# Optimization experiments

Hardware: AMD Instinct MI355X
Metric: run time of the kernel (lower is better)

## Reference

```python
import jax, jax.numpy as jnp
import numpy as np

E = 384      # hidden_dim
H = 8        # num_attention_heads
D = E // H   # head_dim = 48


def setup_inputs() -> dict:
    key = jax.random.key(0)
    ks = jax.random.split(key, 11)
    B, S = 4, 2048
    patch_embeds = jax.random.normal(ks[0], (B, S, E), dtype=jnp.float32)
    attention_mask = jax.random.randint(ks[1], (B, S), 0, 2).astype(bool)
    s = 1.0 / np.sqrt(E)
    Wq = jax.random.normal(ks[2], (E, E), dtype=jnp.float32) * s
    bq = jnp.zeros((E,), dtype=jnp.float32)
    Wk = jax.random.normal(ks[3], (E, E), dtype=jnp.float32) * s
    bk = jnp.zeros((E,), dtype=jnp.float32)
    Wv = jax.random.normal(ks[4], (E, E), dtype=jnp.float32) * s
    bv = jnp.zeros((E,), dtype=jnp.float32)
    Wo = jax.random.normal(ks[5], (E, E), dtype=jnp.float32) * s
    bo = jnp.zeros((E,), dtype=jnp.float32)
    return {"patch_embeds": patch_embeds, "attention_mask": attention_mask,
            "Wq": Wq, "bq": bq, "Wk": Wk, "bk": bk,
            "Wv": Wv, "bv": bv, "Wo": Wo, "bo": bo}


def reference(patch_embeds, attention_mask, Wq, bq, Wk, bk, Wv, bv, Wo, bo):
    B, S, _ = patch_embeds.shape
    scale = D ** (-0.5)
    # QKV projections (nn.Linear: x @ W.T + b); W stored as [out,in]
    q = patch_embeds @ Wq.T + bq
    k = patch_embeds @ Wk.T + bk
    v = patch_embeds @ Wv.T + bv
    # [B,S,E] -> [B,H,S,D]
    q = q.reshape(B, S, H, D).transpose(0, 2, 1, 3)
    k = k.reshape(B, S, H, D).transpose(0, 2, 1, 3)
    v = v.reshape(B, S, H, D).transpose(0, 2, 1, 3)
    # scaled dot-product attention with key mask (True = masked)
    scores = jnp.einsum('bhqd,bhkd->bhqk', q, k) * scale
    mask = attention_mask[:, None, None, :]  # [B,1,1,S]
    scores = jnp.where(mask, -jnp.inf, scores)
    weights = jax.nn.softmax(scores, axis=-1)
    out = jnp.einsum('bhqk,bhkd->bhqd', weights, v)
    out = out.transpose(0, 2, 1, 3).reshape(B, S, E)
    return out @ Wo.T + bo
```

## Files before the change

### kernel.cpp

```cpp
#include <hip/hip_runtime.h>
#include <math.h>

#define B_ 4
#define S_ 2048
#define E_ 384
#define H_ 8
#define D_ 48
#define M_ (B_*S_)
#define DP_ 64
constexpr float QK_SCALE = 0.14433756729740643f * 1.4426950408889634f;

typedef __attribute__((ext_vector_type(8))) short short8;
typedef __attribute__((ext_vector_type(4))) float f32x4;
typedef __attribute__((ext_vector_type(4))) unsigned uint4v;
typedef unsigned short u16;

__device__ inline u16 f2bf(float f) {
    unsigned u = __float_as_uint(f);
    return (u16)((u + 0x7FFFu + ((u >> 16) & 1u)) >> 16);
}
__device__ inline float bf2f(u16 h) { return __uint_as_float(((unsigned)h) << 16); }
__device__ inline unsigned pk2(float a, float b) {
    return (unsigned)f2bf(a) | ((unsigned)f2bf(b) << 16);
}
__device__ inline unsigned pk2_fast(float a, float b) {
#if __has_builtin(__builtin_amdgcn_perm)
    unsigned ua = __float_as_uint(a) + 0x8000u;
    unsigned ub = __float_as_uint(b) + 0x8000u;
    return __builtin_amdgcn_perm(ub, ua, 0x07060302u);
#else
    return pk2(a, b);
#endif
}
__device__ inline float fexp2(float x) {
#if __has_builtin(__builtin_amdgcn_exp2f)
    return __builtin_amdgcn_exp2f(x);
#else
    return exp2f(x);
#endif
}
__device__ inline void glld16(const void* g, void* l) {
    __builtin_amdgcn_global_load_lds((const __attribute__((address_space(1))) unsigned int*)g,
                                     (__attribute__((address_space(3))) unsigned int*)l, 16, 0, 0);
}
__device__ inline void plswap32(unsigned &a, unsigned &b) {
#if __has_builtin(__builtin_amdgcn_permlane32_swap)
    auto r = __builtin_amdgcn_permlane32_swap(a, b, false, false);
    a = r[0]; b = r[1];
#else
    asm volatile("v_permlane32_swap_b32 %0, %1" : "+v"(a), "+v"(b));
#endif
}
__device__ inline void plswap16(unsigned &a, unsigned &b) {
#if __has_builtin(__builtin_amdgcn_permlane16_swap)
    auto r = __builtin_amdgcn_permlane16_swap(a, b, false, false);
    a = r[0]; b = r[1];
#else
    asm volatile("v_permlane16_swap_b32 %0, %1" : "+v"(a), "+v"(b));
#endif
}

__global__ __launch_bounds__(256) void prep(const float4* __restrict__ x,
                                            const int* __restrict__ mask,
                                            const float4* __restrict__ wq,
                                            const float4* __restrict__ wk,
                                            const float4* __restrict__ wv,
                                            const float4* __restrict__ wo,
                                            uint2* __restrict__ xb,
                                            uint2* __restrict__ wb,
                                            u16* __restrict__ Qp, u16* __restrict__ Kp) {
    const int bx = blockIdx.x, t = threadIdx.x;
    if (bx < 3072) {
        int i = bx * 256 + t;
        float4 v = x[i];
        uint2 H;
        H.x = pk2(v.x, v.y);
        H.y = pk2(v.z, v.w);
        xb[i] = H;
    } else if (bx < 3072 + 144) {
        int i = (bx - 3072) * 256 + t;
        const int n4 = 36864;
        const float4* srcs[4] = {wq, wk, wv, wo};
        #pragma unroll
        for (int j = 0; j < 4; ++j) {
            float4 v = srcs[j][i];
            uint2 H;
            H.x = pk2(v.x, v.y);
            H.y = pk2(v.z, v.w);
            wb[(size_t)j * n4 + i] = H;
        }
    } else {
        int i = (bx - 3216) * 256 + t;
        int bh = i >> 11, s = i & 2047, b = bh >> 3;
        size_t off = ((size_t)bh * S_ + s) * DP_ + 48;
        uint4 qz = {0x00004300u, 0, 0, 0};
        uint4 kz = {mask[b * S_ + s] ? 0x0000BF80u : 0u, 0, 0, 0};
        uint4 z  = {0, 0, 0, 0};
        *reinterpret_cast<uint4*>(Qp + off)     = qz;
        *reinterpret_cast<uint4*>(Qp + off + 8) = z;
        *reinterpret_cast<uint4*>(Kp + off)     = kz;
        *reinterpret_cast<uint4*>(Kp + off + 8) = z;
    }
}

__global__ __launch_bounds__(256) void gemm_qkv3(const u16* __restrict__ xb,
                                                 const u16* __restrict__ wb,
                                                 const float* __restrict__ bq,
                                                 const float* __restrict__ bk,
                                                 const float* __restrict__ bv,
                                                 u16* __restrict__ Qp, u16* __restrict__ Kp,
                                                 u16* __restrict__ Vtp) {
    __shared__ u16 smem[4 * 4096];
    u16* As = smem;

    const int t = threadIdx.x, w = t >> 6, lane = t & 63;
    const int ln = lane & 15, quad = lane >> 4;
    const int gr = lane >> 3;
    const int gc = (lane & 7) ^ gr;
    const int m0 = blockIdx.x * 64;
    const int n0 = blockIdx.y * 64;
    const int b  = m0 >> 11;

    f32x4 acc[3][4];
    #pragma unroll
    for (int j = 0; j < 3; ++j)
        #pragma unroll
        for (int nt = 0; nt < 4; ++nt)
            acc[j][nt] = (f32x4){0.f, 0.f, 0.f, 0.f};

    for (int kk = 0; kk < 384; kk += 64) {
        __syncthreads();
        #pragma unroll
        for (int i = 0; i < 2; ++i) {
            int r0 = w * 16 + i * 8;
            glld16(xb + (size_t)(m0 + r0 + gr) * E_ + kk + gc * 8, As + r0 * 64);
        }
        #pragma unroll
        for (int j = 0; j < 3; ++j)
            #pragma unroll
            for (int i = 0; i < 2; ++i) {
                int r0 = w * 16 + i * 8;
                glld16(wb + (size_t)j * 147456 + (size_t)(n0 + r0 + gr) * E_ + kk + gc * 8,
                       smem + (1 + j) * 4096 + r0 * 64);
            }
        __syncthreads();

        #pragma unroll
        for (int ks = 0; ks < 2; ++ks) {
            const int slot = (ks * 4 + quad) ^ (ln & 7);
            short8 ah = *reinterpret_cast<const short8*>(&As[(w * 16 + ln) * 64 + slot * 8]);
            #pragma unroll
            for (int j = 0; j < 3; ++j) {
                const u16* Wsj = smem + (1 + j) * 4096;
                #pragma unroll
                for (int nt = 0; nt < 4; ++nt) {
                    short8 wf = *reinterpret_cast<const short8*>(&Wsj[(nt * 16 + ln) * 64 + slot * 8]);
                    acc[j][nt] = __builtin_amdgcn_mfma_f32_16x16x32_bf16(ah, wf, acc[j][nt], 0, 0, 0);
                }
            }
        }
    }

    {
        const int s_base = (m0 & 2047) + w * 16 + quad * 4;
        #pragma unroll
        for (int nt = 0; nt < 4; ++nt) {
            const int col = n0 + nt * 16 + ln;
            const int h   = (col * 683) >> 15;
            const int d   = col - h * 48;
            const float bc = bv[col];
            u16* dst = Vtp + ((size_t)(b * 8 + h) * 48 + d) * 2048;
            uint2 pk;
            pk.x = pk2(acc[2][nt][0] + bc, acc[2][nt][1] + bc);
            pk.y = pk2(acc[2][nt][2] + bc, acc[2][nt][3] + bc);
            *reinterpret_cast<uint2*>(dst + s_base) = pk;
        }
    }

    u16* TrQ = smem;
    u16* TrK = smem + 64 * 76;
    __syncthreads();
    #pragma unroll
    for (int nt = 0; nt < 4; ++nt) {
        const int col = n0 + nt * 16 + ln;
        const float bcq = bq[col], bck = bk[col];
        #pragma unroll
        for (int r = 0; r < 4; ++r) {
            int row = w * 16 + quad * 4 + r;
            TrQ[row * 76 + nt * 16 + ln] = f2bf((acc[0][nt][r] + bcq) * QK_SCALE);
            TrK[row * 76 + nt * 16 + ln] = f2bf(acc[1][nt][r] + bck);
        }
    }
    __syncthreads();
    {
        const int row = t >> 2, quarter = t & 3;
        const int s   = (m0 & 2047) + row;
        #pragma unroll
        for (int c = 0; c < 2; ++c) {
            int gcol = n0 + quarter * 16 + c * 8;
            int h = (gcol * 683) >> 15;
            int d = gcol - h * 48;
            size_t off = ((size_t)(b * 8 + h) * 2048 + s) * DP_ + d;
            *reinterpret_cast<uint4*>(Qp + off) =
                *reinterpret_cast<const uint4*>(&TrQ[row * 76 + quarter * 16 + c * 8]);
            *reinterpret_cast<uint4*>(Kp + off) =
                *reinterpret_cast<const uint4*>(&TrK[row * 76 + quarter * 16 + c * 8]);
        }
    }
}

__global__ __launch_bounds__(256) void gemm_out(const u16* __restrict__ ab,
                                                const u16* __restrict__ wb,
                                                const float* __restrict__ bo, float* __restrict__ out) {
    __shared__ u16 smem[2 * 4096 + 2 * 4096];
    u16* As = smem;
    u16* Ws = smem + 2 * 4096;
    const int t = threadIdx.x, w = t >> 6, lane = t & 63;
    const int ln = lane & 15, quad = lane >> 4;
    const int gr = lane >> 3;
    const int gc = (lane & 7) ^ gr;
    const int m0 = blockIdx.x * 64, n0 = blockIdx.y * 64;
    const u16* wh = wb + (size_t)3 * 147456;

    f32x4 acc[4];
    #pragma unroll
    for (int nt = 0; nt < 4; ++nt) acc[nt] = (f32x4){0.f, 0.f, 0.f, 0.f};

    auto stage = [&](int bf, int kk) {
        #pragma unroll
        for (int i = 0; i < 2; ++i) {
            int r0 = w * 16 + i * 8;
            glld16(ab + (size_t)(m0 + r0 + gr) * E_ + kk + gc * 8, As + bf * 4096 + r0 * 64);
            glld16(wh + (size_t)(n0 + r0 + gr) * E_ + kk + gc * 8, Ws + bf * 4096 + r0 * 64);
        }
    };

    stage(0, 0);
    __syncthreads();
    #pragma unroll
    for (int it = 0; it < 6; ++it) {
        const int cur = it & 1;
        if (it < 5) stage(cur ^ 1, (it + 1) * 64);
        const u16* Ab = As + cur * 4096;
        const u16* Wb = Ws + cur * 4096;
        #pragma unroll
        for (int ks = 0; ks < 2; ++ks) {
            const int slot = (ks * 4 + quad) ^ (ln & 7);
            short8 ah = *reinterpret_cast<const short8*>(&Ab[(w * 16 + ln) * 64 + slot * 8]);
            #pragma unroll
            for (int nt = 0; nt < 4; ++nt) {
                short8 wf = *reinterpret_cast<const short8*>(&Wb[(nt * 16 + ln) * 64 + slot * 8]);
                acc[nt] = __builtin_amdgcn_mfma_f32_16x16x32_bf16(ah, wf, acc[nt], 0, 0, 0);
            }
        }
        __syncthreads();
    }

    #pragma unroll
    for (int nt = 0; nt < 4; ++nt) {
        const int col = n0 + nt * 16 + ln;
        const float bc = bo[col];
        #pragma unroll
        for (int r = 0; r < 4; ++r) {
            size_t row = (size_t)(m0 + w * 16 + quad * 4 + r);
            out[row * E_ + col] = acc[nt][r] + bc;
        }
    }
}

__global__ __launch_bounds__(512, 4) void attn_mfma(const u16* __restrict__ Qp,
                                                    const u16* __restrict__ Kp,
                                                    const u16* __restrict__ Vtp,
                                                    u16* __restrict__ AO) {
    __shared__ __align__(16) u16 QPs[128 * 64];
    __shared__ __align__(16) u16 Ksh[2][128 * 64];
    __shared__ __align__(16) u16 Vt[2][48 * 128];
    __shared__ float linv[8][16];

    const int t    = threadIdx.x;
    const int w    = t >> 6;
    const int lane = t & 63;
    const int ln   = lane & 15;
    const int quad = lane >> 4;
    const int gr   = lane >> 3;
    const int gc   = (lane & 7) ^ gr;
    const int vr   = lane >> 4;
    const int vc   = lane & 15;
    const int bh   = blockIdx.x;
    const int q0   = blockIdx.y * 128;
    const int b    = bh >> 3, h = bh & 7;
    const int cb   = h * 48;
    const size_t rb = (size_t)b * S_;

    const u16* Qsrc = Qp  + ((size_t)bh * S_ + q0) * DP_;
    const u16* Ksrc = Kp  + (size_t)bh * S_ * DP_;
    const u16* Vsrc = Vtp + (size_t)bh * 48 * 2048;

    const int swz0 = ((quad    ) ^ (ln & 7)) << 3;
    const int swz1 = ((4 + quad) ^ (ln & 7)) << 3;
    const u16* kA[2][2];
    const u16* vA[2][4];
    #pragma unroll
    for (int bf = 0; bf < 2; ++bf) {
        kA[bf][0] = &Ksh[bf][ln * 64 + swz0];
        kA[bf][1] = &Ksh[bf][ln * 64 + swz1];
        #pragma unroll
        for (int g = 0; g < 4; ++g)
            vA[bf][g] = &Vt[bf][ln * 128 + (((g * 4 + quad) ^ (ln & 7)) << 3)];
    }
    const int qrow = (w * 16 + ln) * 64;
    const u16* pR[2];
    pR[0] = &QPs[qrow + swz0];
    pR[1] = &QPs[qrow + swz1];

    auto stage = [&](int bf, int kt) {
        const int k0 = kt * 128;
        #pragma unroll
        for (int i = 0; i < 2; ++i)
            glld16(Ksrc + (size_t)(k0 + w * 16 + i * 8 + gr) * DP_ + gc * 8,
                   &Ksh[bf][(w * 16 + i * 8) * 64]);
        if (w < 6) {
            #pragma unroll
            for (int j = 0; j < 2; ++j) {
                const int vrow = w * 8 + j * 4 + vr;
                glld16(Vsrc + (size_t)vrow * 2048 + k0 + (vc ^ (vrow & 7)) * 8,
                       &Vt[bf][(w * 8 + j * 4) * 128]);
            }
        }
    };

    #pragma unroll
    for (int i = 0; i < 2; ++i) {
        int r0 = w * 16 + i * 8;
        glld16(Qsrc + (size_t)(r0 + gr) * DP_ + gc * 8, &QPs[r0 * 64]);
    }
    stage(0, 0);
    __syncthreads();

    short8 qf[2];
    qf[0] = *reinterpret_cast<const short8*>(pR[0]);
    qf[1] = *reinterpret_cast<const short8*>(pR[1]);

    f32x4 o[3];
    #pragma unroll
    for (int nt = 0; nt < 3; ++nt) o[nt] = (f32x4){0.f, 0.f, 0.f, 0.f};
    float lq = 0.f;

    auto body = [&](int cur, int nxt, int ktn) {
        if (ktn < 16) stage(nxt, ktn);

        short8 pa[4];
        #pragma unroll
        for (int hf = 0; hf < 2; ++hf) {
            f32x4 sc[4];
            #pragma unroll
            for (int m = 0; m < 4; ++m) {
                const int Mt = hf * 4 + m;
                short8 kf0 = *reinterpret_cast<const short8*>(kA[cur][0] + Mt * 1024);
                short8 kf1 = *reinterpret_cast<const short8*>(kA[cur][1] + Mt * 1024);
                f32x4 a0 = __builtin_amdgcn_mfma_f32_16x16x32_bf16(kf0, qf[0], (f32x4){0.f,0.f,0.f,0.f}, 0, 0, 0);
                sc[m] = __builtin_amdgcn_mfma_f32_16x16x32_bf16(kf1, qf[1], a0, 0, 0, 0);
            }
            unsigned U[4][2];
            #pragma unroll
            for (int m = 0; m < 4; ++m) {
                float p0 = fexp2(sc[m][0]);
                float p1 = fexp2(sc[m][1]);
                float p2 = fexp2(sc[m][2]);
                float p3 = fexp2(sc[m][3]);
                lq += (p0 + p1) + (p2 + p3);
                U[m][0] = pk2_fast(p0, p1);
                U[m][1] = pk2_fast(p2, p3);
            }
            #pragma unroll
            for (int g = 0; g < 2; ++g) {
                unsigned a0 = U[g * 2][0], b0 = U[g * 2 + 1][0];
                plswap32(a0, b0); plswap16(a0, b0);
                unsigned a1 = U[g * 2][1], b1 = U[g * 2 + 1][1];
                plswap32(a1, b1); plswap16(a1, b1);
                uint4v uv = {a0, a1, b0, b1};
                pa[hf * 2 + g] = __builtin_bit_cast(short8, uv);
            }
        }

        #pragma unroll
        for (int nt = 0; nt < 3; ++nt)
            #pragma unroll
            for (int g = 0; g < 4; ++g) {
                short8 vb = *reinterpret_cast<const short8*>(vA[cur][g] + nt * 2048);
                o[nt] = __builtin_amdgcn_mfma_f32_16x16x32_bf16(pa[g], vb, o[nt], 0, 0, 0);
            }
        __syncthreads();
    };

    for (int kt = 0; kt < 16; kt += 2) {
        body(0, 1, kt + 1);
        body(1, 0, kt + 2);
    }

    {
        float l = lq;
        l += __shfl_xor(l, 16);
        l += __shfl_xor(l, 32);
        if (quad == 0) linv[w][ln] = 1.0f / l;
    }
    __syncthreads();
    {
        f32x4 il = *reinterpret_cast<const f32x4*>(&linv[w][quad * 4]);
        #pragma unroll
        for (int nt = 0; nt < 3; ++nt)
            #pragma unroll
            for (int r = 0; r < 4; ++r) {
                size_t row = rb + q0 + w * 16 + quad * 4 + r;
                size_t idx = row * E_ + cb + nt * 16 + ln;
                AO[idx] = f2bf(o[nt][r] * il[r]);
            }
    }
}

extern "C" void kernel_launch(void* const* d_in, const int* in_sizes, int n_in,
                              void* d_out, int out_size, void* d_ws, size_t ws_size,
                              hipStream_t stream) {
    (void)in_sizes; (void)n_in; (void)out_size; (void)ws_size;
    const float* x    = (const float*)d_in[0];
    const int*   mask = (const int*)  d_in[1];
    const float* Wq   = (const float*)d_in[2];
    const float* bq   = (const float*)d_in[3];
    const float* Wk   = (const float*)d_in[4];
    const float* bk   = (const float*)d_in[5];
    const float* Wv   = (const float*)d_in[6];
    const float* bv   = (const float*)d_in[7];
    const float* Wo   = (const float*)d_in[8];
    const float* bo   = (const float*)d_in[9];

    const size_t NELEM = (size_t)M_ * E_;
    const size_t WELEM = (size_t)E_ * E_;
    const size_t PEL   = (size_t)B_ * H_ * S_ * DP_;
    u16* ws = (u16*)d_ws;
    u16* xb  = ws;
    u16* wb  = xb + NELEM;
    u16* Qp  = wb + 4 * WELEM;
    u16* Kp  = Qp + PEL;
    u16* Vtp = Kp + PEL;
    u16* AO  = xb;

    dim3 blk(256);
    prep<<<dim3(3472), blk, 0, stream>>>(
        (const float4*)x, mask,
        (const float4*)Wq, (const float4*)Wk, (const float4*)Wv, (const float4*)Wo,
        (uint2*)xb, (uint2*)wb, Qp, Kp);

    gemm_qkv3<<<dim3(M_ / 64, 6), blk, 0, stream>>>(xb, wb, bq, bk, bv, Qp, Kp, Vtp);

    attn_mfma<<<dim3(B_ * H_, S_ / 128), dim3(512), 0, stream>>>(Qp, Kp, Vtp, AO);

    gemm_out<<<dim3(M_ / 64, 6), blk, 0, stream>>>(AO, wb, bo, (float*)d_out);
}
```

Measured before the change: 146.1 us.

## Prefetch QKV GEMM tiles via registers and split attention V tile into halves

The QKV projection GEMM now issues the global loads for the next K-slab into registers before running the MFMAs on the current slab, then writes them to LDS. This replaces the synchronous global-to-LDS loads so memory latency overlaps with compute. The attention kernel stores each V tile as two 64-column halves, which makes the V staging match the same 8-row swizzled pattern used for K and changes how the V fragments are addressed. The trade-offs are more register pressure in the GEMM and an extra barrier per iteration.

```diff
diff --git a/kernel.cpp b/kernel.cpp
--- a/kernel.cpp
+++ b/kernel.cpp
@@ -121,6 +121,11 @@
     const int n0 = blockIdx.y * 64;
     const int b  = m0 >> 11;
 
+    const u16* aSrc = xb + (size_t)(m0 + w * 16 + gr) * E_ + gc * 8;
+    const u16* wSrc0 = wb + (size_t)0 * 147456 + (size_t)(n0 + w * 16 + gr) * E_ + gc * 8;
+    const u16* wSrc1 = wb + (size_t)1 * 147456 + (size_t)(n0 + w * 16 + gr) * E_ + gc * 8;
+    const u16* wSrc2 = wb + (size_t)2 * 147456 + (size_t)(n0 + w * 16 + gr) * E_ + gc * 8;
+
     f32x4 acc[3][4];
     #pragma unroll
     for (int j = 0; j < 3; ++j)
@@ -128,22 +133,35 @@
         for (int nt = 0; nt < 4; ++nt)
             acc[j][nt] = (f32x4){0.f, 0.f, 0.f, 0.f};
 
-    for (int kk = 0; kk < 384; kk += 64) {
-        __syncthreads();
+    short8 rA0, rA1, rW[3][2];
+    auto loads = [&](int kk) {
+        rA0 = *reinterpret_cast<const short8*>(aSrc + kk);
+        rA1 = *reinterpret_cast<const short8*>(aSrc + 8 * E_ + kk);
         #pragma unroll
         for (int i = 0; i < 2; ++i) {
-            int r0 = w * 16 + i * 8;
-            glld16(xb + (size_t)(m0 + r0 + gr) * E_ + kk + gc * 8, As + r0 * 64);
-        }
+            rW[0][i] = *reinterpret_cast<const short8*>(wSrc0 + i * 8 * E_ + kk);
+            rW[1][i] = *reinterpret_cast<const short8*>(wSrc1 + i * 8 * E_ + kk);
+            rW[2][i] = *reinterpret_cast<const short8*>(wSrc2 + i * 8 * E_ + kk);
+        }
+    };
+    auto writes = [&]() {
+        *reinterpret_cast<short8*>(As + (w * 16) * 64 + lane * 8)     = rA0;
+        *reinterpret_cast<short8*>(As + (w * 16 + 8) * 64 + lane * 8) = rA1;
         #pragma unroll
         for (int j = 0; j < 3; ++j)
             #pragma unroll
-            for (int i = 0; i < 2; ++i) {
-                int r0 = w * 16 + i * 8;
-                glld16(wb + (size_t)j * 147456 + (size_t)(n0 + r0 + gr) * E_ + kk + gc * 8,
-                       smem + (1 + j) * 4096 + r0 * 64);
-            }
-        __syncthreads();
+            for (int i = 0; i < 2; ++i)
+                *reinterpret_cast<short8*>(smem + (1 + j) * 4096 +
+                                           (w * 16 + i * 8) * 64 + lane * 8) = rW[j][i];
+    };
+
+    loads(0);
+    writes();
+    __syncthreads();
+
+    #pragma unroll
+    for (int it = 0; it < 6; ++it) {
+        if (it < 5) loads((it + 1) * 64);
 
         #pragma unroll
         for (int ks = 0; ks < 2; ++ks) {
@@ -158,6 +176,11 @@
                     acc[j][nt] = __builtin_amdgcn_mfma_f32_16x16x32_bf16(ah, wf, acc[j][nt], 0, 0, 0);
                 }
             }
+        }
+        __syncthreads();
+        if (it < 5) {
+            writes();
+            __syncthreads();
         }
     }
 
@@ -274,7 +297,7 @@
                                                     u16* __restrict__ AO) {
     __shared__ __align__(16) u16 QPs[128 * 64];
     __shared__ __align__(16) u16 Ksh[2][128 * 64];
-    __shared__ __align__(16) u16 Vt[2][48 * 128];
+    __shared__ __align__(16) u16 Vt[2][2][48 * 64];
     __shared__ float linv[8][16];
 
     const int t    = threadIdx.x;
@@ -284,8 +307,6 @@
     const int quad = lane >> 4;
     const int gr   = lane >> 3;
     const int gc   = (lane & 7) ^ gr;
-    const int vr   = lane >> 4;
-    const int vc   = lane & 15;
     const int bh   = blockIdx.x;
     const int q0   = blockIdx.y * 128;
     const int b    = bh >> 3, h = bh & 7;
@@ -306,7 +327,7 @@
         kA[bf][1] = &Ksh[bf][ln * 64 + swz1];
         #pragma unroll
         for (int g = 0; g < 4; ++g)
-            vA[bf][g] = &Vt[bf][ln * 128 + (((g * 4 + quad) ^ (ln & 7)) << 3)];
+            vA[bf][g] = &Vt[bf][g >> 1][ln * 64 + ((((g & 1) * 4 + quad) ^ (ln & 7)) << 3)];
     }
     const int qrow = (w * 16 + ln) * 64;
     const u16* pR[2];
@@ -320,12 +341,8 @@
             glld16(Ksrc + (size_t)(k0 + w * 16 + i * 8 + gr) * DP_ + gc * 8,
                    &Ksh[bf][(w * 16 + i * 8) * 64]);
         if (w < 6) {
-            #pragma unroll
-            for (int j = 0; j < 2; ++j) {
-                const int vrow = w * 8 + j * 4 + vr;
-                glld16(Vsrc + (size_t)vrow * 2048 + k0 + (vc ^ (vrow & 7)) * 8,
-                       &Vt[bf][(w * 8 + j * 4) * 128]);
-            }
+            glld16(Vsrc + (size_t)(w * 8 + gr) * 2048 + k0 + gc * 8,      &Vt[bf][0][(w * 8) * 64]);
+            glld16(Vsrc + (size_t)(w * 8 + gr) * 2048 + k0 + 64 + gc * 8, &Vt[bf][1][(w * 8) * 64]);
         }
     };
 
@@ -387,7 +404,7 @@
         for (int nt = 0; nt < 3; ++nt)
             #pragma unroll
             for (int g = 0; g < 4; ++g) {
-                short8 vb = *reinterpret_cast<const short8*>(vA[cur][g] + nt * 2048);
+                short8 vb = *reinterpret_cast<const short8*>(vA[cur][g] + nt * 1024);
                 o[nt] = __builtin_amdgcn_mfma_f32_16x16x32_bf16(pa[g], vb, o[nt], 0, 0, 0);
             }
         __syncthreads();
```

Result: no change. 146.7 us (+0.4%).
